# Performance work log

Measured on AMD Instinct MI355X. Metric: run time of the kernel, lower is better.

The kernel has to match this reference:

```python
import jax, jax.numpy as jnp
import numpy as np

N = 100000   # nodes
E = 800000   # edges
F_IN = 64    # num_node_features
H = 64       # hidden_channels
C = 10       # num_classes


def setup_inputs() -> dict:
    key = jax.random.key(0)
    ks = jax.random.split(key, 12)
    def w(k, fan_in, fan_out):
        return (jax.random.normal(k, (fan_in, fan_out), jnp.float32)
                / np.sqrt(fan_in).astype(np.float32))
    x = jax.random.normal(ks[0], (N, F_IN), jnp.float32)
    edge_index = jax.random.randint(ks[1], (2, E), 0, N, dtype=jnp.int32).astype(jnp.int64)
    return {
        "x": x,
        "edge_index": edge_index,
        # GraphConv 1: lin_rel (with bias) on aggregated, lin_root (no bias) on x
        "W1_rel": w(ks[2], F_IN, H), "b1": jnp.zeros((H,), jnp.float32), "W1_root": w(ks[3], F_IN, H),
        # GraphConv 2
        "W2_rel": w(ks[4], H, H), "b2": jnp.zeros((H,), jnp.float32), "W2_root": w(ks[5], H, H),
        # GCNConv 3
        "W3": w(ks[6], H, H), "b3": jnp.zeros((H,), jnp.float32),
        # final Linear head
        "Wlin": w(ks[7], H, C), "blin": jnp.zeros((C,), jnp.float32),
    }


def _graph_conv(x, src, dst, W_rel, b_rel, W_root):
    # PyG GraphConv (aggr='add'): out = W_rel @ sum_{j->i} x_j + b_rel + W_root @ x_i
    agg = jax.ops.segment_sum(x[src], dst, num_segments=N)  # [N, F] scatter-add
    return agg @ W_rel + b_rel + x @ W_root


def _gcn_conv(x, src, dst, W, b):
    # PyG GCNConv: add self-loops, symmetric norm D^-1/2 (A+I) D^-1/2, then X W + b
    xw = x @ W
    loops = jnp.arange(N, dtype=src.dtype)
    src2 = jnp.concatenate([src, loops])
    dst2 = jnp.concatenate([dst, loops])
    deg = jax.ops.segment_sum(jnp.ones_like(dst2, dtype=xw.dtype), dst2, num_segments=N)
    dinv = jax.lax.rsqrt(deg)  # deg >= 1 thanks to self-loops
    norm = dinv[src2] * dinv[dst2]  # [E+N]
    out = jax.ops.segment_sum(xw[src2] * norm[:, None], dst2, num_segments=N)
    return out + b


def reference(x, edge_index, W1_rel, b1, W1_root, W2_rel, b2, W2_root, W3, b3, Wlin, blin):
    src, dst = edge_index[0], edge_index[1]
    h = jax.nn.relu(_graph_conv(x, src, dst, W1_rel, b1, W1_root))
    h = jax.nn.relu(_graph_conv(h, src, dst, W2_rel, b2, W2_root))
    h = _gcn_conv(h, src, dst, W3, b3)
    # task='node_classification' -> no pooling; dropout is identity in eval mode
    return h @ Wlin + blin
```

## Files before the change

kernel.cpp:

```cpp
#include <hip/hip_runtime.h>

#define NN 100000
#define NE 800000
#define BSH 9
#define BSZ (1 << BSH)
#define NBUK ((NN + BSZ - 1) / BSZ)
#define NCHUNK 196
#define CAPB 64
#define CAP_C 7168

typedef _Float16 half8 __attribute__((ext_vector_type(8)));
typedef float f32x4 __attribute__((ext_vector_type(4)));

__global__ __launch_bounds__(256) void k_setup(
    const float* __restrict__ W1r, const float* __restrict__ W1o,
    const float* __restrict__ W2r, const float* __restrict__ W2o,
    const float* __restrict__ W3, const float* __restrict__ b3,
    const float* __restrict__ Wlin, const float* __restrict__ blin,
    const float* __restrict__ x, const int* __restrict__ ei,
    _Float16* __restrict__ W12, _Float16* __restrict__ W34h,
    float* __restrict__ cvec,
    _Float16* __restrict__ xh, _Float16* __restrict__ Ah, _Float16* __restrict__ P,
    int* __restrict__ cnt2, int* __restrict__ ebuf2)
{
  const int m = blockIdx.x, tid = threadIdx.x;

  if (m >= 3129) {
    __shared__ int curs[256];
    const int c = m - 3129;
    curs[tid] = 0;
    __syncthreads();
    const int e0 = c * 4096;
    int pk[16], bk[16];
#pragma unroll
    for (int i = 0; i < 16; ++i) {
      int e = e0 + i * 256 + tid;
      if (e < NE) {
        int src = ei[e];
        int dst = ei[NE + e];
        bk[i] = dst >> BSH;
        pk[i] = src | ((dst & (BSZ - 1)) << 17);
      } else bk[i] = -1;
    }
#pragma unroll
    for (int i = 0; i < 16; ++i) {
      if (bk[i] >= 0) {
        int slot = atomicAdd(&curs[bk[i]], 1);
        ebuf2[(c * NBUK + bk[i]) * CAPB + slot] = pk[i];
      }
    }
    __syncthreads();
    if (tid < NBUK) cnt2[c * NBUK + tid] = curs[tid];
    return;
  }

  if (m >= 4) {
    int idx = (m - 4) * 256 + tid;
    const float4* p4 = (const float4*)(x + idx * 8);
    float4 a = p4[0], b = p4[1];
    half8 h;
    h[0] = (_Float16)a.x; h[1] = (_Float16)a.y; h[2] = (_Float16)a.z; h[3] = (_Float16)a.w;
    h[4] = (_Float16)b.x; h[5] = (_Float16)b.y; h[6] = (_Float16)b.z; h[7] = (_Float16)b.w;
    *(half8*)(xh + idx * 8) = h;
    return;
  }

  if (m < 2) {
    const float* Wr = m ? W2r : W1r;
    const float* Wo = m ? W2o : W1o;
    _Float16* dst = W12 + m * 8192;
    for (int idx = tid; idx < 8192; idx += 256) {
      int n = idx >> 7, k = idx & 127;
      float v = (k < 64) ? Wr[k * 64 + n] : Wo[(k - 64) * 64 + n];
      dst[idx] = (_Float16)v;
    }
  } else if (m == 2) {
    for (int idx = tid; idx < 1024; idx += 256) {
      int c = idx >> 6, k = idx & 63;
      float s = 0.f;
      if (c < 10)
        for (int j = 0; j < 64; ++j) s = fmaf(W3[k * 64 + j], Wlin[j * 10 + c], s);
      W34h[idx] = (_Float16)s;
    }
    if (tid < 10) {
      float s = blin[tid];
      for (int j = 0; j < 64; ++j) s = fmaf(b3[j], Wlin[j * 10 + tid], s);
      cvec[tid] = s;
    }
  } else {
    if (tid < 64) {
      xh[NN * 64 + tid] = (_Float16)0.f;
      Ah[NN * 64 + tid] = (_Float16)0.f;
    }
    if (tid < 16) P[NN * 16 + tid] = (_Float16)0.f;
  }
}

__global__ __launch_bounds__(256) void k_csr2(const int* __restrict__ cnt2,
    const int* __restrict__ ebuf2, int2* __restrict__ rp2, int* __restrict__ csr,
    float* __restrict__ dinv)
{
  __shared__ int stage[6144];
  __shared__ int h[BSZ];
  __shared__ int loff[BSZ];
  __shared__ int cur[BSZ];
  __shared__ int sd[256];
  __shared__ int cbase[NCHUNK];
  __shared__ int ntot;
  const int tid = threadIdx.x;
  const int b = blockIdx.x;
  h[tid] = 0; h[tid + 256] = 0;

  int v = (tid < NCHUNK) ? cnt2[tid * NBUK + b] : 0;
  sd[tid] = v;
  __syncthreads();
  int incl = v;
  for (int o = 1; o < 256; o <<= 1) {
    int add = (tid >= o) ? sd[tid - o] : 0;
    __syncthreads();
    incl += add;
    sd[tid] = incl;
    __syncthreads();
  }
  if (tid < NCHUNK) cbase[tid] = incl - v;
  if (tid == 255) ntot = incl;
  __syncthreads();

  if (tid < NCHUNK) {
    const int* src = ebuf2 + (tid * NBUK + b) * CAPB;
    int base = cbase[tid];
    for (int i = 0; i < v; ++i) stage[base + i] = src[i];
  }
  __syncthreads();
  const int n = ntot;

  for (int i = tid; i < n; i += 256)
    atomicAdd(&h[stage[i] >> 17], 1);
  __syncthreads();

  int r0 = h[2 * tid], r1 = h[2 * tid + 1];
  int p0 = (r0 + 7) & ~7, p1 = (r1 + 7) & ~7;
  int ps = p0 + p1;
  sd[tid] = ps;
  __syncthreads();
  int incl2 = ps;
  for (int o = 1; o < 256; o <<= 1) {
    int add = (tid >= o) ? sd[tid - o] : 0;
    __syncthreads();
    incl2 += add;
    sd[tid] = incl2;
    __syncthreads();
  }
  int ex = incl2 - ps;
  loff[2 * tid] = ex;
  loff[2 * tid + 1] = ex + p0;
  cur[2 * tid] = ex;
  cur[2 * tid + 1] = ex + p0;
  __syncthreads();

  const int node0 = b * BSZ;
  const int cbase2 = b * CAP_C;
#pragma unroll
  for (int t = 0; t < 2; ++t) {
    int j = tid + t * 256;
    int node = node0 + j;
    if (node < NN) {
      int hr = h[j];
      int hp = (hr + 7) & ~7;
      int beg = cbase2 + loff[j];
      rp2[node] = make_int2(beg, beg + hp);
      dinv[node] = rsqrtf((float)hr + 1.0f);
      for (int p = hr; p < hp; ++p) csr[beg + p] = NN;
    }
  }

  for (int i = tid; i < n; i += 256) {
    int w = stage[i];
    int dl = w >> 17;
    int slot = atomicAdd(&cur[dl], 1);
    csr[cbase2 + slot] = w & 0x1FFFF;
  }
}

template<bool PSTAGE>
__global__ __launch_bounds__(512) void k_layer(
    const _Float16* __restrict__ Ain, const int2* __restrict__ rp2,
    const int* __restrict__ csr, const _Float16* __restrict__ W12,
    const float* __restrict__ bias, const float* __restrict__ dinv,
    _Float16* __restrict__ Aout, const _Float16* __restrict__ W34h,
    _Float16* __restrict__ P)
{
  __shared__ _Float16 sW[64 * 128];
  __shared__ _Float16 sA[128 * 128];
  __shared__ _Float16 sW34[PSTAGE ? 16 * 64 : 8];

  const int tid = threadIdx.x;
  const int node0 = blockIdx.x * 128;
  const int l = tid & 63, w = tid >> 6;

  {
    const uint4* g4 = (const uint4*)W12;
#pragma unroll
    for (int i = 0; i < 2; ++i) {
      int c = tid + 512 * i;
      int n = c >> 4, kc = c & 15;
      *(uint4*)((char*)sW + n * 256 + ((kc * 16) ^ ((n & 7) << 4))) = g4[c];
    }
    if (PSTAGE && tid < 128) {
      int n = tid >> 3, kc = tid & 7;
      uint4 v = ((const uint4*)W34h)[tid];
      *(uint4*)((char*)sW34 + n * 128 + ((kc * 16) ^ ((n & 7) << 4))) = v;
    }
  }

  const int grp = l >> 3, c8 = l & 7;
#pragma unroll
  for (int r = 0; r < 2; ++r) {
    int nl = r * 64 + w * 8 + grp;
    int node = node0 + nl;
    float acc[8];
#pragma unroll
    for (int j = 0; j < 8; ++j) acc[j] = 0.f;
    half8 selfv = {};
    if (node < NN) {
      int2 se = rp2[node];
      for (int i = se.x; i < se.y; i += 8) {
        int4 sa = *(const int4*)(csr + i);
        int4 sb = *(const int4*)(csr + i + 4);
        half8 v0 = *(const half8*)(Ain + sa.x * 64 + c8 * 8);
        half8 v1 = *(const half8*)(Ain + sa.y * 64 + c8 * 8);
        half8 v2 = *(const half8*)(Ain + sa.z * 64 + c8 * 8);
        half8 v3 = *(const half8*)(Ain + sa.w * 64 + c8 * 8);
        half8 v4 = *(const half8*)(Ain + sb.x * 64 + c8 * 8);
        half8 v5 = *(const half8*)(Ain + sb.y * 64 + c8 * 8);
        half8 v6 = *(const half8*)(Ain + sb.z * 64 + c8 * 8);
        half8 v7 = *(const half8*)(Ain + sb.w * 64 + c8 * 8);
#pragma unroll
        for (int j = 0; j < 8; ++j)
          acc[j] += (((float)v0[j] + (float)v1[j]) + ((float)v2[j] + (float)v3[j]))
                  + (((float)v4[j] + (float)v5[j]) + ((float)v6[j] + (float)v7[j]));
      }
      selfv = *(const half8*)(Ain + node * 64 + c8 * 8);
    }
    half8 ha;
#pragma unroll
    for (int j = 0; j < 8; ++j) ha[j] = (_Float16)acc[j];
    char* rowp = (char*)sA + nl * 256;
    int swz = (nl & 7) << 4;
    *(half8*)(rowp + ((c8 * 16) ^ swz)) = ha;
    *(half8*)(rowp + ((128 + c8 * 16) ^ swz)) = selfv;
  }
  __syncthreads();

  const int lm = l & 15, lh = l >> 4;
  f32x4 acc[4];
#pragma unroll
  for (int nt = 0; nt < 4; ++nt) acc[nt] = (f32x4){0.f, 0.f, 0.f, 0.f};

  const int arow = w * 16 + lm;
  const int aswz = (arow & 7) << 4;
#pragma unroll
  for (int kb = 0; kb < 4; ++kb) {
    half8 af = *(half8*)((char*)sA + arow * 256 + ((kb * 64 + lh * 16) ^ aswz));
#pragma unroll
    for (int nt = 0; nt < 4; ++nt) {
      int n = nt * 16 + lm;
      half8 bf = *(half8*)((char*)sW + n * 256 + ((kb * 64 + lh * 16) ^ ((n & 7) << 4)));
      acc[nt] = __builtin_amdgcn_mfma_f32_16x16x32_f16(af, bf, acc[nt], 0, 0, 0);
    }
  }

  if (!PSTAGE) {
#pragma unroll
    for (int nt = 0; nt < 4; ++nt) {
      int col = nt * 16 + lm;
      float bv = bias[col];
#pragma unroll
      for (int r2 = 0; r2 < 4; ++r2) {
        int row = node0 + w * 16 + lh * 4 + r2;
        if (row < NN)
          Aout[row * 64 + col] = (_Float16)fmaxf(acc[nt][r2] + bv, 0.f);
      }
    }
  } else {
#pragma unroll
    for (int r2 = 0; r2 < 4; ++r2) {
      int lrow = w * 16 + lh * 4 + r2;
      int grow = node0 + lrow;
      float s = (grow < NN) ? dinv[grow] : 0.f;
      char* rowp = (char*)sA + lrow * 256;
      int swz = (lrow & 7) << 4;
#pragma unroll
      for (int nt = 0; nt < 4; ++nt) {
        int col = nt * 16 + lm;
        float v = fmaxf(acc[nt][r2] + bias[col], 0.f) * s;
        *(_Float16*)(rowp + ((col * 2) ^ swz)) = (_Float16)v;
      }
    }
    f32x4 accP = (f32x4){0.f, 0.f, 0.f, 0.f};
#pragma unroll
    for (int kb = 0; kb < 2; ++kb) {
      half8 af = *(half8*)((char*)sA + arow * 256 + ((kb * 64 + lh * 16) ^ aswz));
      half8 bf = *(half8*)((char*)sW34 + lm * 128 + ((kb * 64 + lh * 16) ^ ((lm & 7) << 4)));
      accP = __builtin_amdgcn_mfma_f32_16x16x32_f16(af, bf, accP, 0, 0, 0);
    }
#pragma unroll
    for (int r2 = 0; r2 < 4; ++r2) {
      int row = node0 + w * 16 + lh * 4 + r2;
      if (row < NN) P[row * 16 + lm] = (_Float16)accP[r2];
    }
  }
}

__global__ __launch_bounds__(256) void k_head2(const int2* __restrict__ rp2,
    const int* __restrict__ csr, const _Float16* __restrict__ P,
    const float* __restrict__ dinv, const float* __restrict__ cvecg,
    float* __restrict__ out)
{
  __shared__ float sc[10];
  const int tid = threadIdx.x;
  if (tid < 10) sc[tid] = cvecg[tid];
  __syncthreads();

  const int node = blockIdx.x * 128 + (tid >> 1);
  const int half = tid & 1;
  if (node >= NN) return;
  int2 se = rp2[node];

  float acc[8];
#pragma unroll
  for (int j = 0; j < 8; ++j) acc[j] = 0.f;

  for (int i = se.x; i < se.y; i += 8) {
    int4 sa = *(const int4*)(csr + i);
    int4 sb = *(const int4*)(csr + i + 4);
    half8 v0 = *(const half8*)(P + sa.x * 16 + half * 8);
    half8 v1 = *(const half8*)(P + sa.y * 16 + half * 8);
    half8 v2 = *(const half8*)(P + sa.z * 16 + half * 8);
    half8 v3 = *(const half8*)(P + sa.w * 16 + half * 8);
    half8 v4 = *(const half8*)(P + sb.x * 16 + half * 8);
    half8 v5 = *(const half8*)(P + sb.y * 16 + half * 8);
    half8 v6 = *(const half8*)(P + sb.z * 16 + half * 8);
    half8 v7 = *(const half8*)(P + sb.w * 16 + half * 8);
#pragma unroll
    for (int j = 0; j < 8; ++j)
      acc[j] += (((float)v0[j] + (float)v1[j]) + ((float)v2[j] + (float)v3[j]))
              + (((float)v4[j] + (float)v5[j]) + ((float)v6[j] + (float)v7[j]));
  }
  half8 selfv = *(const half8*)(P + node * 16 + half * 8);
#pragma unroll
  for (int j = 0; j < 8; ++j) acc[j] += (float)selfv[j];

  float dv = dinv[node];
  if (half == 0) {
#pragma unroll
    for (int j = 0; j < 4; ++j) {
      float2 o;
      o.x = fmaf(dv, acc[2 * j], sc[2 * j]);
      o.y = fmaf(dv, acc[2 * j + 1], sc[2 * j + 1]);
      *(float2*)(out + node * 10 + 2 * j) = o;
    }
  } else {
    float2 o;
    o.x = fmaf(dv, acc[0], sc[8]);
    o.y = fmaf(dv, acc[1], sc[9]);
    *(float2*)(out + node * 10 + 8) = o;
  }
}

extern "C" void kernel_launch(void* const* d_in, const int* in_sizes, int n_in,
                              void* d_out, int out_size, void* d_ws, size_t ws_size,
                              hipStream_t stream) {
  const float* x       = (const float*)d_in[0];
  const int*   ei      = (const int*)d_in[1];
  const float* W1_rel  = (const float*)d_in[2];
  const float* b1      = (const float*)d_in[3];
  const float* W1_root = (const float*)d_in[4];
  const float* W2_rel  = (const float*)d_in[5];
  const float* b2      = (const float*)d_in[6];
  const float* W2_root = (const float*)d_in[7];
  const float* W3      = (const float*)d_in[8];
  const float* b3      = (const float*)d_in[9];
  const float* Wlin    = (const float*)d_in[10];
  const float* blin    = (const float*)d_in[11];
  float* out = (float*)d_out;

  char* ws = (char*)d_ws;
  _Float16* xh   = (_Float16*)(ws);
  _Float16* Ah   = (_Float16*)(ws + 12800128);
  float*    dinv = (float*)(ws + 25600256);
  int2*     rp2  = (int2*) (ws + 26000256);
  int*      csr  = (int*)  (ws + 26800256);
  _Float16* W12  = (_Float16*)(ws + 32419968);
  _Float16* W34h = (_Float16*)(ws + 32452736);
  float*    cvec = (float*)(ws + 32454784);
  _Float16* P    = (_Float16*)(ws + 32454848);
  int*      cnt2 = (int*)  (ws + 35654880);
  int*      ebuf2= (int*)  (ws + 35808544);

  dim3 b256(256), b512(512);

  k_setup<<<3325, b256, 0, stream>>>(W1_rel, W1_root, W2_rel, W2_root, W3, b3, Wlin,
                                     blin, x, ei, W12, W34h, cvec, xh, Ah, P,
                                     cnt2, ebuf2);
  k_csr2<<<NBUK, b256, 0, stream>>>(cnt2, ebuf2, rp2, csr, dinv);

  const int gl = (NN + 127) / 128;

  k_layer<false><<<gl, b512, 0, stream>>>(xh, rp2, csr, W12, b1, nullptr, Ah,
                                          nullptr, nullptr);
  k_layer<true><<<gl, b512, 0, stream>>>(Ah, rp2, csr, W12 + 8192, b2, dinv, nullptr,
                                         W34h, P);
  k_head2<<<gl, b256, 0, stream>>>(rp2, csr, P, dinv, cvec, out);
}
```

Baseline: 96.76 us.

## Pad CSR rows to four and spread head gather across eight lanes per node

CSR rows are now padded to a multiple of 4 instead of 8, which cuts the dummy neighbor reads. The layer kernels gain a 4-wide tail loop to handle the new padding. The final head kernel now gives each node 8 lanes instead of 2: each lane gathers one neighbor half-row and the partial sums are combined with xor shuffles, which raises memory-level parallelism on short rows. The trade-off is more blocks (3125) and shuffle overhead, plus extra branching in the layer tail.

```diff
diff --git a/kernel.cpp b/kernel.cpp
--- a/kernel.cpp
+++ b/kernel.cpp
@@ -139,7 +139,7 @@
   __syncthreads();
 
   int r0 = h[2 * tid], r1 = h[2 * tid + 1];
-  int p0 = (r0 + 7) & ~7, p1 = (r1 + 7) & ~7;
+  int p0 = (r0 + 3) & ~3, p1 = (r1 + 3) & ~3;
   int ps = p0 + p1;
   sd[tid] = ps;
   __syncthreads();
@@ -166,7 +166,7 @@
     int node = node0 + j;
     if (node < NN) {
       int hr = h[j];
-      int hp = (hr + 7) & ~7;
+      int hp = (hr + 3) & ~3;
       int beg = cbase2 + loff[j];
       rp2[node] = make_int2(beg, beg + hp);
       dinv[node] = rsqrtf((float)hr + 1.0f);
@@ -224,7 +224,8 @@
     half8 selfv = {};
     if (node < NN) {
       int2 se = rp2[node];
-      for (int i = se.x; i < se.y; i += 8) {
+      int i = se.x;
+      for (; i + 8 <= se.y; i += 8) {
         int4 sa = *(const int4*)(csr + i);
         int4 sb = *(const int4*)(csr + i + 4);
         half8 v0 = *(const half8*)(Ain + sa.x * 64 + c8 * 8);
@@ -240,6 +241,16 @@
           acc[j] += (((float)v0[j] + (float)v1[j]) + ((float)v2[j] + (float)v3[j]))
                   + (((float)v4[j] + (float)v5[j]) + ((float)v6[j] + (float)v7[j]));
       }
+      if (i < se.y) {
+        int4 sa = *(const int4*)(csr + i);
+        half8 v0 = *(const half8*)(Ain + sa.x * 64 + c8 * 8);
+        half8 v1 = *(const half8*)(Ain + sa.y * 64 + c8 * 8);
+        half8 v2 = *(const half8*)(Ain + sa.z * 64 + c8 * 8);
+        half8 v3 = *(const half8*)(Ain + sa.w * 64 + c8 * 8);
+#pragma unroll
+        for (int j = 0; j < 8; ++j)
+          acc[j] += ((float)v0[j] + (float)v1[j]) + ((float)v2[j] + (float)v3[j]);
+      }
       selfv = *(const half8*)(Ain + node * 64 + c8 * 8);
     }
     half8 ha;
@@ -322,49 +333,49 @@
   if (tid < 10) sc[tid] = cvecg[tid];
   __syncthreads();
 
-  const int node = blockIdx.x * 128 + (tid >> 1);
-  const int half = tid & 1;
-  if (node >= NN) return;
+  const int l = tid & 63, w = tid >> 6;
+  const int grp = l >> 3, c = l & 7;
+  const int j2 = c >> 1, hf = c & 1;
+  const int node = blockIdx.x * 32 + w * 8 + grp;
   int2 se = rp2[node];
 
   float acc[8];
 #pragma unroll
   for (int j = 0; j < 8; ++j) acc[j] = 0.f;
 
-  for (int i = se.x; i < se.y; i += 8) {
-    int4 sa = *(const int4*)(csr + i);
-    int4 sb = *(const int4*)(csr + i + 4);
-    half8 v0 = *(const half8*)(P + sa.x * 16 + half * 8);
-    half8 v1 = *(const half8*)(P + sa.y * 16 + half * 8);
-    half8 v2 = *(const half8*)(P + sa.z * 16 + half * 8);
-    half8 v3 = *(const half8*)(P + sa.w * 16 + half * 8);
-    half8 v4 = *(const half8*)(P + sb.x * 16 + half * 8);
-    half8 v5 = *(const half8*)(P + sb.y * 16 + half * 8);
-    half8 v6 = *(const half8*)(P + sb.z * 16 + half * 8);
-    half8 v7 = *(const half8*)(P + sb.w * 16 + half * 8);
-#pragma unroll
-    for (int j = 0; j < 8; ++j)
-      acc[j] += (((float)v0[j] + (float)v1[j]) + ((float)v2[j] + (float)v3[j]))
-              + (((float)v4[j] + (float)v5[j]) + ((float)v6[j] + (float)v7[j]));
-  }
-  half8 selfv = *(const half8*)(P + node * 16 + half * 8);
-#pragma unroll
-  for (int j = 0; j < 8; ++j) acc[j] += (float)selfv[j];
-
-  float dv = dinv[node];
-  if (half == 0) {
-#pragma unroll
-    for (int j = 0; j < 4; ++j) {
+  for (int i = se.x; i < se.y; i += 4) {
+    int4 ss = *(const int4*)(csr + i);
+    int s = (j2 == 0) ? ss.x : (j2 == 1) ? ss.y : (j2 == 2) ? ss.z : ss.w;
+    half8 v = *(const half8*)(P + s * 16 + hf * 8);
+#pragma unroll
+    for (int j = 0; j < 8; ++j) acc[j] += (float)v[j];
+  }
+
+#pragma unroll
+  for (int j = 0; j < 8; ++j) {
+    acc[j] += __shfl_xor(acc[j], 2);
+    acc[j] += __shfl_xor(acc[j], 4);
+  }
+
+  if (c < 2) {
+    half8 selfv = *(const half8*)(P + node * 16 + hf * 8);
+#pragma unroll
+    for (int j = 0; j < 8; ++j) acc[j] += (float)selfv[j];
+    float dv = dinv[node];
+    if (c == 0) {
+#pragma unroll
+      for (int j = 0; j < 4; ++j) {
+        float2 o;
+        o.x = fmaf(dv, acc[2 * j], sc[2 * j]);
+        o.y = fmaf(dv, acc[2 * j + 1], sc[2 * j + 1]);
+        *(float2*)(out + node * 10 + 2 * j) = o;
+      }
+    } else {
       float2 o;
-      o.x = fmaf(dv, acc[2 * j], sc[2 * j]);
-      o.y = fmaf(dv, acc[2 * j + 1], sc[2 * j + 1]);
-      *(float2*)(out + node * 10 + 2 * j) = o;
-    }
-  } else {
-    float2 o;
-    o.x = fmaf(dv, acc[0], sc[8]);
-    o.y = fmaf(dv, acc[1], sc[9]);
-    *(float2*)(out + node * 10 + 8) = o;
+      o.x = fmaf(dv, acc[0], sc[8]);
+      o.y = fmaf(dv, acc[1], sc[9]);
+      *(float2*)(out + node * 10 + 8) = o;
+    }
   }
 }
 
@@ -411,5 +422,5 @@
                                           nullptr, nullptr);
   k_layer<true><<<gl, b512, 0, stream>>>(Ah, rp2, csr, W12 + 8192, b2, dinv, nullptr,
                                          W34h, P);
-  k_head2<<<gl, b256, 0, stream>>>(rp2, csr, P, dinv, cvec, out);
+  k_head2<<<3125, b256, 0, stream>>>(rp2, csr, P, dinv, cvec, out);
 }
```

Result: slower. 102.0 us (+5.5%).

## Fuse two GNN layers and head into one cooperative persistent kernel

Applied to the files above, without the earlier changes.

Replaces the three separate launches (layer 1, layer 2, head) with a single cooperative kernel that loops over tiles persistently and uses grid-wide syncs between phases. Weights are staged into shared memory once per block per phase instead of once per tile. The intent is to remove launch gaps and tail effects between kernels. In exchange, the grid is capped by occupancy, grid.sync adds its own cost, and the head phase now runs 512 threads per 256-node tile.

```diff
diff --git a/kernel.cpp b/kernel.cpp
--- a/kernel.cpp
+++ b/kernel.cpp
@@ -1,4 +1,6 @@
 #include <hip/hip_runtime.h>
+#include <hip/hip_cooperative_groups.h>
+namespace cg = cooperative_groups;
 
 #define NN 100000
 #define NE 800000
@@ -8,6 +10,8 @@
 #define NCHUNK 196
 #define CAPB 64
 #define CAP_C 7168
+#define NTILE 782
+#define NHTILE 391
 
 typedef _Float16 half8 __attribute__((ext_vector_type(8)));
 typedef float f32x4 __attribute__((ext_vector_type(4)));
@@ -183,37 +187,17 @@
 }
 
 template<bool PSTAGE>
-__global__ __launch_bounds__(512) void k_layer(
-    const _Float16* __restrict__ Ain, const int2* __restrict__ rp2,
-    const int* __restrict__ csr, const _Float16* __restrict__ W12,
-    const float* __restrict__ bias, const float* __restrict__ dinv,
-    _Float16* __restrict__ Aout, const _Float16* __restrict__ W34h,
-    _Float16* __restrict__ P)
+__device__ __forceinline__ void layer_tile(
+    int tile, const _Float16* __restrict__ Ain, const int2* __restrict__ rp2,
+    const int* __restrict__ csr, const float* __restrict__ bias,
+    const float* __restrict__ dinv, _Float16* __restrict__ Aout,
+    _Float16* __restrict__ P, _Float16* sW, _Float16* sA, _Float16* sW34)
 {
-  __shared__ _Float16 sW[64 * 128];
-  __shared__ _Float16 sA[128 * 128];
-  __shared__ _Float16 sW34[PSTAGE ? 16 * 64 : 8];
-
   const int tid = threadIdx.x;
-  const int node0 = blockIdx.x * 128;
+  const int node0 = tile * 128;
   const int l = tid & 63, w = tid >> 6;
-
-  {
-    const uint4* g4 = (const uint4*)W12;
-#pragma unroll
-    for (int i = 0; i < 2; ++i) {
-      int c = tid + 512 * i;
-      int n = c >> 4, kc = c & 15;
-      *(uint4*)((char*)sW + n * 256 + ((kc * 16) ^ ((n & 7) << 4))) = g4[c];
-    }
-    if (PSTAGE && tid < 128) {
-      int n = tid >> 3, kc = tid & 7;
-      uint4 v = ((const uint4*)W34h)[tid];
-      *(uint4*)((char*)sW34 + n * 128 + ((kc * 16) ^ ((n & 7) << 4))) = v;
-    }
-  }
-
   const int grp = l >> 3, c8 = l & 7;
+
 #pragma unroll
   for (int r = 0; r < 2; ++r) {
     int nl = r * 64 + w * 8 + grp;
@@ -310,61 +294,105 @@
       if (row < NN) P[row * 16 + lm] = (_Float16)accP[r2];
     }
   }
+  __syncthreads();
 }
 
-__global__ __launch_bounds__(256) void k_head2(const int2* __restrict__ rp2,
-    const int* __restrict__ csr, const _Float16* __restrict__ P,
-    const float* __restrict__ dinv, const float* __restrict__ cvecg,
-    float* __restrict__ out)
+__global__ __launch_bounds__(512) void k_gnn(
+    const _Float16* __restrict__ xh, _Float16* __restrict__ Ah,
+    const int2* __restrict__ rp2, const int* __restrict__ csr,
+    const _Float16* __restrict__ W12, const float* __restrict__ b1,
+    const float* __restrict__ b2, const float* __restrict__ dinv,
+    const _Float16* __restrict__ W34h, _Float16* __restrict__ P,
+    const float* __restrict__ cvecg, float* __restrict__ out)
 {
+  cg::grid_group grid = cg::this_grid();
+  __shared__ _Float16 sW[64 * 128];
+  __shared__ _Float16 sA[128 * 128];
+  __shared__ _Float16 sW34[16 * 64];
   __shared__ float sc[10];
+
   const int tid = threadIdx.x;
+
+  {
+    const uint4* g4 = (const uint4*)W12;
+#pragma unroll
+    for (int i = 0; i < 2; ++i) {
+      int c = tid + 512 * i;
+      int n = c >> 4, kc = c & 15;
+      *(uint4*)((char*)sW + n * 256 + ((kc * 16) ^ ((n & 7) << 4))) = g4[c];
+    }
+  }
+  for (int t = blockIdx.x; t < NTILE; t += gridDim.x)
+    layer_tile<false>(t, xh, rp2, csr, b1, nullptr, Ah, nullptr, sW, sA, sW34);
+
+  grid.sync();
+
+  {
+    const uint4* g4 = (const uint4*)(W12 + 8192);
+#pragma unroll
+    for (int i = 0; i < 2; ++i) {
+      int c = tid + 512 * i;
+      int n = c >> 4, kc = c & 15;
+      *(uint4*)((char*)sW + n * 256 + ((kc * 16) ^ ((n & 7) << 4))) = g4[c];
+    }
+    if (tid < 128) {
+      int n = tid >> 3, kc = tid & 7;
+      uint4 v = ((const uint4*)W34h)[tid];
+      *(uint4*)((char*)sW34 + n * 128 + ((kc * 16) ^ ((n & 7) << 4))) = v;
+    }
+  }
+  for (int t = blockIdx.x; t < NTILE; t += gridDim.x)
+    layer_tile<true>(t, Ah, rp2, csr, b2, dinv, nullptr, P, sW, sA, sW34);
+
+  grid.sync();
+
   if (tid < 10) sc[tid] = cvecg[tid];
   __syncthreads();
-
-  const int node = blockIdx.x * 128 + (tid >> 1);
-  const int half = tid & 1;
-  if (node >= NN) return;
-  int2 se = rp2[node];
-
-  float acc[8];
-#pragma unroll
-  for (int j = 0; j < 8; ++j) acc[j] = 0.f;
-
-  for (int i = se.x; i < se.y; i += 8) {
-    int4 sa = *(const int4*)(csr + i);
-    int4 sb = *(const int4*)(csr + i + 4);
-    half8 v0 = *(const half8*)(P + sa.x * 16 + half * 8);
-    half8 v1 = *(const half8*)(P + sa.y * 16 + half * 8);
-    half8 v2 = *(const half8*)(P + sa.z * 16 + half * 8);
-    half8 v3 = *(const half8*)(P + sa.w * 16 + half * 8);
-    half8 v4 = *(const half8*)(P + sb.x * 16 + half * 8);
-    half8 v5 = *(const half8*)(P + sb.y * 16 + half * 8);
-    half8 v6 = *(const half8*)(P + sb.z * 16 + half * 8);
-    half8 v7 = *(const half8*)(P + sb.w * 16 + half * 8);
-#pragma unroll
-    for (int j = 0; j < 8; ++j)
-      acc[j] += (((float)v0[j] + (float)v1[j]) + ((float)v2[j] + (float)v3[j]))
-              + (((float)v4[j] + (float)v5[j]) + ((float)v6[j] + (float)v7[j]));
-  }
-  half8 selfv = *(const half8*)(P + node * 16 + half * 8);
-#pragma unroll
-  for (int j = 0; j < 8; ++j) acc[j] += (float)selfv[j];
-
-  float dv = dinv[node];
-  if (half == 0) {
-#pragma unroll
-    for (int j = 0; j < 4; ++j) {
+  for (int t = blockIdx.x; t < NHTILE; t += gridDim.x) {
+    int node = t * 256 + (tid >> 1);
+    int half = tid & 1;
+    if (node >= NN) continue;
+    int2 se = rp2[node];
+
+    float acc[8];
+#pragma unroll
+    for (int j = 0; j < 8; ++j) acc[j] = 0.f;
+
+    for (int i = se.x; i < se.y; i += 8) {
+      int4 sa = *(const int4*)(csr + i);
+      int4 sb = *(const int4*)(csr + i + 4);
+      half8 v0 = *(const half8*)(P + sa.x * 16 + half * 8);
+      half8 v1 = *(const half8*)(P + sa.y * 16 + half * 8);
+      half8 v2 = *(const half8*)(P + sa.z * 16 + half * 8);
+      half8 v3 = *(const half8*)(P + sa.w * 16 + half * 8);
+      half8 v4 = *(const half8*)(P + sb.x * 16 + half * 8);
+      half8 v5 = *(const half8*)(P + sb.y * 16 + half * 8);
+      half8 v6 = *(const half8*)(P + sb.z * 16 + half * 8);
+      half8 v7 = *(const half8*)(P + sb.w * 16 + half * 8);
+#pragma unroll
+      for (int j = 0; j < 8; ++j)
+        acc[j] += (((float)v0[j] + (float)v1[j]) + ((float)v2[j] + (float)v3[j]))
+                + (((float)v4[j] + (float)v5[j]) + ((float)v6[j] + (float)v7[j]));
+    }
+    half8 selfv = *(const half8*)(P + node * 16 + half * 8);
+#pragma unroll
+    for (int j = 0; j < 8; ++j) acc[j] += (float)selfv[j];
+
+    float dv = dinv[node];
+    if (half == 0) {
+#pragma unroll
+      for (int j = 0; j < 4; ++j) {
+        float2 o;
+        o.x = fmaf(dv, acc[2 * j], sc[2 * j]);
+        o.y = fmaf(dv, acc[2 * j + 1], sc[2 * j + 1]);
+        *(float2*)(out + node * 10 + 2 * j) = o;
+      }
+    } else {
       float2 o;
-      o.x = fmaf(dv, acc[2 * j], sc[2 * j]);
-      o.y = fmaf(dv, acc[2 * j + 1], sc[2 * j + 1]);
-      *(float2*)(out + node * 10 + 2 * j) = o;
-    }
-  } else {
-    float2 o;
-    o.x = fmaf(dv, acc[0], sc[8]);
-    o.y = fmaf(dv, acc[1], sc[9]);
-    *(float2*)(out + node * 10 + 8) = o;
+      o.x = fmaf(dv, acc[0], sc[8]);
+      o.y = fmaf(dv, acc[1], sc[9]);
+      *(float2*)(out + node * 10 + 8) = o;
+    }
   }
 }
 
@@ -405,11 +433,20 @@
                                      cnt2, ebuf2);
   k_csr2<<<NBUK, b256, 0, stream>>>(cnt2, ebuf2, rp2, csr, dinv);
 
-  const int gl = (NN + 127) / 128;
-
-  k_layer<false><<<gl, b512, 0, stream>>>(xh, rp2, csr, W12, b1, nullptr, Ah,
-                                          nullptr, nullptr);
-  k_layer<true><<<gl, b512, 0, stream>>>(Ah, rp2, csr, W12 + 8192, b2, dinv, nullptr,
-                                         W34h, P);
-  k_head2<<<gl, b256, 0, stream>>>(rp2, csr, P, dinv, cvec, out);
+  int dev = 0;
+  hipGetDevice(&dev);
+  int ncu = 256;
+  hipDeviceGetAttribute(&ncu, hipDeviceAttributeMultiprocessorCount, dev);
+  int maxb = 1;
+  hipOccupancyMaxActiveBlocksPerMultiprocessor(&maxb, (const void*)k_gnn, 512, 0);
+  if (maxb < 1) maxb = 1;
+  int grid = maxb * ncu;
+  if (grid > NTILE) grid = NTILE;
+
+  void* args[] = {
+    (void*)&xh, (void*)&Ah, (void*)&rp2, (void*)&csr, (void*)&W12,
+    (void*)&b1, (void*)&b2, (void*)&dinv, (void*)&W34h, (void*)&P,
+    (void*)&cvec, (void*)&out
+  };
+  hipLaunchCooperativeKernel((const void*)k_gnn, dim3(grid), b512, args, 0, stream);
 }
```

Result: slower. 191.2 us (+97.6%).
